# Performance work log

Measured on AMD Instinct MI355X. Metric: run time of the kernel, lower is better.

Reference implementation:

```python
import jax, jax.numpy as jnp
import numpy as np

N_NODES = 110
C = 4096  # in_channels = hidden = out_channels


def setup_inputs() -> dict:
    key = jax.random.key(0)
    ks = jax.random.split(key, 8)
    x = jax.random.normal(ks[0], (N_NODES, C), dtype=jnp.float32)
    adj = jax.random.randint(ks[1], (N_NODES, N_NODES), 0, 2, dtype=jnp.int32)
    # torch.nn.Linear weights stored [out_features, in_features]
    W2 = jax.random.normal(ks[2], (C, C), dtype=jnp.float32) / np.sqrt(C)
    b2 = jax.random.normal(ks[3], (C,), dtype=jnp.float32) * 0.01
    W1 = jax.random.normal(ks[4], (2 * C, C), dtype=jnp.float32) / np.sqrt(2 * C)
    b1 = jax.random.normal(ks[5], (C,), dtype=jnp.float32) * 0.01
    Wl = jax.random.normal(ks[6], (N_NODES, N_NODES), dtype=jnp.float32) / np.sqrt(N_NODES)
    bl = jax.random.normal(ks[7], (N_NODES,), dtype=jnp.float32) * 0.01
    # note: W1 is stored [in=2C, out=C]; W2 [in=C, out=C]; Wl [in=110, out=110]
    return {"x": x, "adj": adj, "W2": W2, "b2": b2, "W1": W1, "b1": b1, "Wl": Wl, "bl": bl}


def reference(x, adj, W2, b2, W1, b1, Wl, bl):
    # FeatGraphConv: h = lin2(x)
    h = x @ W2 + b2  # [N, C]
    # edge_index.nonzero(): adjacency -> edge list (i=src, j=dst); mean-aggregate
    # h[src] at dst. Dense equivalent: column-normalized mask matmul.
    mask = (adj != 0).astype(x.dtype)  # [N, N]
    deg = mask.sum(axis=0)  # in-degree of each target node j
    aggr = (mask.T @ h) / jnp.maximum(deg, 1.0)[:, None]  # [N, C]; 0 for isolated nodes (PyG mean)
    # update: lin1(cat(h, aggr)) then relu (in RegGNN.forward)
    out = jax.nn.relu(jnp.concatenate([h, aggr], axis=1) @ W1 + b1)  # [N, C]
    # x.t(); lin(110,110); x.t()
    out = (out.T @ Wl.T + bl).T  # [N, C]
    return out
```

## Files before the change

kernel.cpp:

```cpp
#include <hip/hip_runtime.h>
#include <hip/hip_fp16.h>

#define C 4096
#define NN 110
#define MPAD 112
#define NMT 7
#define KBS (NMT * 512)
#define NSLICE 8

typedef _Float16 f16x8 __attribute__((ext_vector_type(8)));
typedef float fx4 __attribute__((ext_vector_type(4)));
typedef unsigned long long ull;


__global__ __launch_bounds__(256)
void prep1_kernel(const float* __restrict__ x, _Float16* __restrict__ A1t) {
    int u = blockIdx.x * 256 + threadIdx.x;
    int kb  = u / 448;
    int rem = u - kb * 448;
    int mt  = rem >> 6;
    int L   = rem & 63;
    int n   = mt * 16 + (L & 15);
    int c   = kb * 32 + (L >> 4) * 8;
    f16x8 hv;
    if (n < NN) {
        float4 v0 = *(const float4*)(x + (size_t)n * C + c);
        float4 v1 = *(const float4*)(x + (size_t)n * C + c + 4);
        hv[0]=(_Float16)v0.x; hv[1]=(_Float16)v0.y; hv[2]=(_Float16)v0.z; hv[3]=(_Float16)v0.w;
        hv[4]=(_Float16)v1.x; hv[5]=(_Float16)v1.y; hv[6]=(_Float16)v1.z; hv[7]=(_Float16)v1.w;
    } else {
        for (int e = 0; e < 8; ++e) hv[e] = (_Float16)0.f;
    }
    *(f16x8*)(A1t + (size_t)u * 8) = hv;
}

__global__ __launch_bounds__(128)
void maskprep_kernel(const int* __restrict__ adj, ull* __restrict__ mlo,
                     ull* __restrict__ mhi, float* __restrict__ degs) {
    int j = threadIdx.x;
    if (j < NN) {
        ull lo = 0, hi = 0; int dg = 0;
        for (int i = 0; i < 64; ++i) {
            int m = (adj[i * NN + j] != 0);
            lo |= ((ull)m) << i; dg += m;
        }
        for (int i = 64; i < NN; ++i) {
            int m = (adj[i * NN + j] != 0);
            hi |= ((ull)m) << (i - 64); dg += m;
        }
        mlo[j] = lo; mhi[j] = hi;
        degs[j] = (float)(dg > 0 ? dg : 1);
    }
}

#define PIPE_BARRIER()                                                \
    do {                                                              \
        asm volatile("s_waitcnt lgkmcnt(0)" ::: "memory");            \
        __builtin_amdgcn_s_barrier();                                 \
        __builtin_amdgcn_sched_barrier(0);                            \
    } while (0)

template<int NITER>
__global__ __launch_bounds__(256, 3)
void mm_kernel(const _Float16* __restrict__ A, const float* __restrict__ B,
               float* __restrict__ Cpart) {
    __shared__ __align__(16) _Float16 As[2][2 * KBS];
    __shared__ __align__(16) _Float16 Bs[2][64 * 64];

    const int t   = threadIdx.x;
    const int j0  = blockIdx.x * 64;
    const int w   = t >> 6;
    const int L   = t & 63;
    const int l15 = L & 15;
    const int q   = L >> 4;
    const int sc2 = (t & 31) * 2;
    const int kgr = (t >> 5) & 7;

    fx4 acc[7];
#pragma unroll
    for (int mt = 0; mt < 7; ++mt) acc[mt] = (fx4){0.f, 0.f, 0.f, 0.f};

    const float*    Bp  = B + (size_t)blockIdx.y * (NITER * 64) * C + j0 + sc2;
    const _Float16* ApC = A + (size_t)blockIdx.y * (NITER * 2) * KBS;
    const _Float16* BsR = &Bs[0][0] + (w * 16 + l15) * 64;
    const _Float16* AsR = &As[0][0];

    f16x8  av[4];
    float2 bva[8], bvb[8];

#define LOADA(ch)                                                              \
    { _Pragma("unroll")                                                        \
      for (int i = 0; i < 4; ++i)                                              \
          if (i < 3 || t < 128)                                                \
              av[i] = *(const f16x8*)(ApC + (size_t)(ch) * (2 * KBS)           \
                                      + (t + i * 256) * 8); }

#define COMMITA(buf)                                                           \
    { _Pragma("unroll")                                                        \
      for (int i = 0; i < 4; ++i)                                              \
          if (i < 3 || t < 128)                                                \
              *(f16x8*)(&As[buf][0] + (t + i * 256) * 8) = av[i]; }

#define LOADB(dst, ch)                                                         \
    { _Pragma("unroll")                                                        \
      for (int p = 0; p < 8; ++p)                                              \
          dst[p] = *(const float2*)(Bp + (size_t)((ch) * 64 + kgr * 8 + p) * C); }

#define COMMITB(src, buf)                                                      \
    { f16x8 h0, h1;                                                            \
      _Pragma("unroll")                                                        \
      for (int e = 0; e < 8; ++e) { h0[e] = (_Float16)src[e].x;                \
                                    h1[e] = (_Float16)src[e].y; }              \
      *(f16x8*)(&Bs[buf][0] + sc2 * 64 + ((kgr ^ (sc2 & 7)) << 3)) = h0;       \
      *(f16x8*)(&Bs[buf][0] + (sc2 + 1) * 64 + ((kgr ^ ((sc2 + 1) & 7)) << 3)) = h1; }

    LOADA(0);
    LOADB(bva, 0);
    COMMITA(0);
    COMMITB(bva, 0);
    LOADB(bva, 1);
    PIPE_BARRIER();

#pragma unroll
    for (int it = 0; it < NITER; ++it) {
        if (it + 1 < NITER) LOADA(it + 1);
        __builtin_amdgcn_sched_barrier(0);
        if (it + 2 < NITER) {
            if (it & 1) { LOADB(bva, it + 2); } else { LOADB(bvb, it + 2); }
        }
        __builtin_amdgcn_sched_barrier(0);
#pragma unroll
        for (int s = 0; s < 2; ++s) {
            f16x8 bf = *(const f16x8*)(BsR + (it & 1) * 4096
                            + ((((s << 2) + q) ^ (l15 & 7)) << 3));
#pragma unroll
            for (int mt = 0; mt < 7; ++mt) {
                f16x8 afrag = *(const f16x8*)(AsR + (it & 1) * (2 * KBS)
                                  + (s * 7 + mt) * 512 + L * 8);
                acc[mt] = __builtin_amdgcn_mfma_f32_16x16x32_f16(
                    afrag, bf, acc[mt], 0, 0, 0);
            }
        }
        if (it + 1 < NITER) {
            COMMITA((it + 1) & 1);
            if (it & 1) { COMMITB(bvb, (it + 1) & 1); }
            else        { COMMITB(bva, (it + 1) & 1); }
            PIPE_BARRIER();
        }
    }

    float* Cp = Cpart + (size_t)blockIdx.y * (NN * C) + j0 + w * 16 + l15;
#pragma unroll
    for (int mt = 0; mt < 7; ++mt)
#pragma unroll
        for (int r = 0; r < 4; ++r) {
            int row = mt * 16 + q * 4 + r;
            if (row < NN)
                Cp[(size_t)row * C] = acc[mt][r];
        }
#undef LOADA
#undef COMMITA
#undef LOADB
#undef COMMITB
}

__device__ __forceinline__ size_t fragidx(int n, int c) {
    return (size_t)(c >> 5) * KBS + (n >> 4) * 512
         + (((c >> 3) & 3) * 16 + (n & 15)) * 8 + (c & 7);
}

__global__ __launch_bounds__(256)
void agg_kernel(const float* __restrict__ hpart, const ull* __restrict__ gmlo,
                const ull* __restrict__ gmhi, const float* __restrict__ gdegs,
                const float* __restrict__ b2, _Float16* __restrict__ A3t) {
    __shared__ float hb[NN * 16];
    const int t  = threadIdx.x;
    const int c0 = blockIdx.x * 16;

    for (int idx = t; idx < NN * 8; idx += 256) {
        int n = idx >> 3, cp = (idx & 7) << 1;
        float v0 = b2[c0 + cp], v1 = b2[c0 + cp + 1];
#pragma unroll
        for (int p = 0; p < NSLICE; ++p) {
            float2 v = *(const float2*)(hpart + (size_t)p * (NN * C)
                                        + (size_t)n * C + c0 + cp);
            v0 += v.x; v1 += v.y;
        }
        hb[n * 16 + cp]     = v0;
        hb[n * 16 + cp + 1] = v1;
        union { _Float16 h[2]; unsigned u; } pk;
        pk.h[0] = (_Float16)v0;
        pk.h[1] = (_Float16)v1;
        *(unsigned*)(A3t + fragidx(n, c0 + cp)) = pk.u;
    }
    if (t < 32) {
        int n  = 110 + ((t >> 3) & 1);
        int hs = t >> 4;
        int cp = (t & 7) << 1;
        *(unsigned*)(A3t + fragidx(n, hs * C + c0 + cp)) = 0u;
    }
    __syncthreads();
    for (int idx = t; idx < NN * 8; idx += 256) {
        int j = idx >> 3, cp = (idx & 7) << 1;
        ull lo = gmlo[j], hi = gmhi[j];
        float dg = gdegs[j];
        float a0 = 0.f, a1 = 0.f;
        for (int i = 0; i < 64; ++i)
            if ((lo >> i) & 1) { a0 += hb[i * 16 + cp]; a1 += hb[i * 16 + cp + 1]; }
        for (int i = 64; i < NN; ++i)
            if ((hi >> (i - 64)) & 1) { a0 += hb[i * 16 + cp]; a1 += hb[i * 16 + cp + 1]; }
        union { _Float16 h[2]; unsigned u; } pk;
        pk.h[0] = (_Float16)(a0 / dg);
        pk.h[1] = (_Float16)(a1 / dg);
        *(unsigned*)(A3t + fragidx(j, C + c0 + cp)) = pk.u;
    }
}

__global__ __launch_bounds__(256)
void zred_kernel(const float* __restrict__ zpart, float* __restrict__ z_raw) {
    int idx = blockIdx.x * 256 + threadIdx.x;
    if (idx < NN * (C / 4)) {
        fx4 s = (fx4){0.f, 0.f, 0.f, 0.f};
#pragma unroll
        for (int p = 0; p < NSLICE; ++p) {
            fx4 v = *(const fx4*)(zpart + (size_t)p * (NN * C) + (size_t)idx * 4);
            s.x += v.x; s.y += v.y; s.z += v.z; s.w += v.w;
        }
        *(fx4*)(z_raw + (size_t)idx * 4) = s;
    }
}

__global__ __launch_bounds__(256)
void fin_kernel(const float* __restrict__ z_raw, const float* __restrict__ b1,
                const float* __restrict__ Wl, const float* __restrict__ bl,
                float* __restrict__ out) {
    __shared__ float zs[NN * 64];
    const int t  = threadIdx.x;
    const int c0 = blockIdx.x * 64;
    const int c  = t & 63;

    for (int idx = t; idx < NN * 64; idx += 256) {
        int k = idx >> 6, cc = idx & 63;
        float v = z_raw[(size_t)k * C + c0 + cc] + b1[c0 + cc];
        zs[idx] = fmaxf(v, 0.f);
    }
    __syncthreads();
    for (int jj = 0; jj < 7; ++jj) {
        int j = blockIdx.y * 28 + jj * 4 + (t >> 6);
        if (j < NN) {
            float a = bl[j];
#pragma unroll 2
            for (int k = 0; k < NN; ++k)
                a += Wl[j * NN + k] * zs[k * 64 + c];
            out[(size_t)j * C + c0 + c] = a;
        }
    }
}

extern "C" void kernel_launch(void* const* d_in, const int* in_sizes, int n_in,
                              void* d_out, int out_size, void* d_ws, size_t ws_size,
                              hipStream_t stream) {
    const float* x   = (const float*)d_in[0];
    const int*   adj = (const int*)d_in[1];
    const float* W2  = (const float*)d_in[2];
    const float* b2  = (const float*)d_in[3];
    const float* W1  = (const float*)d_in[4];
    const float* b1  = (const float*)d_in[5];
    const float* Wl  = (const float*)d_in[6];
    const float* bl  = (const float*)d_in[7];
    float* out = (float*)d_out;

    char* ws = (char*)d_ws;
    float*    hpart = (float*)(ws);
    float*    zpart = (float*)(ws + 14417920);
    float*    z_raw = (float*)(ws + 28835840);
    _Float16* A1t   = (_Float16*)(ws + 30638080);
    _Float16* A3t   = (_Float16*)(ws + 31555584);
    ull*      mlo   = (ull*)(ws + 33390592);
    ull*      mhi   = (ull*)(ws + 33391472);
    float*    degs  = (float*)(ws + 33392352);

    prep1_kernel<<<224, 256, 0, stream>>>(x, A1t);
    maskprep_kernel<<<1, 128, 0, stream>>>(adj, mlo, mhi, degs);
    mm_kernel<8><<<dim3(64, NSLICE), 256, 0, stream>>>(A1t, W2, hpart);
    agg_kernel<<<C / 16, 256, 0, stream>>>(hpart, mlo, mhi, degs, b2, A3t);
    mm_kernel<16><<<dim3(64, NSLICE), 256, 0, stream>>>(A3t, W1, zpart);
    zred_kernel<<<440, 256, 0, stream>>>(zpart, z_raw);
    fin_kernel<<<dim3(C / 64, 4), 256, 0, stream>>>(z_raw, b1, Wl, bl, out);
}
```

Before: 352.1 us.

## Load A fragments directly into registers and fuse mask prep into prep1

The mm kernel no longer stages the A operand through shared memory. Each lane now loads its MFMA A fragments straight from global memory into a double-buffered register array, which removes the LDS writes and reads for A. The launch bound occupancy hint drops from 3 to 2 to make room for the larger register footprint. Separately, the adjacency mask preparation moves into an extra block of prep1, saving one kernel launch. The trade-off is heavier global load traffic per wave, since A fragments are reloaded by each of the 4 waves, plus higher register pressure and possibly lower occupancy.

```diff
diff --git a/kernel.cpp b/kernel.cpp
--- a/kernel.cpp
+++ b/kernel.cpp
@@ -14,7 +14,26 @@
 
 
 __global__ __launch_bounds__(256)
-void prep1_kernel(const float* __restrict__ x, _Float16* __restrict__ A1t) {
+void prep1_kernel(const float* __restrict__ x, _Float16* __restrict__ A1t,
+                  const int* __restrict__ adj, ull* __restrict__ mlo,
+                  ull* __restrict__ mhi, float* __restrict__ degs) {
+    if (blockIdx.x == 224) {
+        int j = threadIdx.x;
+        if (j < NN) {
+            ull lo = 0, hi = 0; int dg = 0;
+            for (int i = 0; i < 64; ++i) {
+                int m = (adj[i * NN + j] != 0);
+                lo |= ((ull)m) << i; dg += m;
+            }
+            for (int i = 64; i < NN; ++i) {
+                int m = (adj[i * NN + j] != 0);
+                hi |= ((ull)m) << (i - 64); dg += m;
+            }
+            mlo[j] = lo; mhi[j] = hi;
+            degs[j] = (float)(dg > 0 ? dg : 1);
+        }
+        return;
+    }
     int u = blockIdx.x * 256 + threadIdx.x;
     int kb  = u / 448;
     int rem = u - kb * 448;
@@ -34,25 +53,6 @@
     *(f16x8*)(A1t + (size_t)u * 8) = hv;
 }
 
-__global__ __launch_bounds__(128)
-void maskprep_kernel(const int* __restrict__ adj, ull* __restrict__ mlo,
-                     ull* __restrict__ mhi, float* __restrict__ degs) {
-    int j = threadIdx.x;
-    if (j < NN) {
-        ull lo = 0, hi = 0; int dg = 0;
-        for (int i = 0; i < 64; ++i) {
-            int m = (adj[i * NN + j] != 0);
-            lo |= ((ull)m) << i; dg += m;
-        }
-        for (int i = 64; i < NN; ++i) {
-            int m = (adj[i * NN + j] != 0);
-            hi |= ((ull)m) << (i - 64); dg += m;
-        }
-        mlo[j] = lo; mhi[j] = hi;
-        degs[j] = (float)(dg > 0 ? dg : 1);
-    }
-}
-
 #define PIPE_BARRIER()                                                \
     do {                                                              \
         asm volatile("s_waitcnt lgkmcnt(0)" ::: "memory");            \
@@ -61,10 +61,9 @@
     } while (0)
 
 template<int NITER>
-__global__ __launch_bounds__(256, 3)
+__global__ __launch_bounds__(256, 2)
 void mm_kernel(const _Float16* __restrict__ A, const float* __restrict__ B,
                float* __restrict__ Cpart) {
-    __shared__ __align__(16) _Float16 As[2][2 * KBS];
     __shared__ __align__(16) _Float16 Bs[2][64 * 64];
 
     const int t   = threadIdx.x;
@@ -81,25 +80,19 @@
     for (int mt = 0; mt < 7; ++mt) acc[mt] = (fx4){0.f, 0.f, 0.f, 0.f};
 
     const float*    Bp  = B + (size_t)blockIdx.y * (NITER * 64) * C + j0 + sc2;
-    const _Float16* ApC = A + (size_t)blockIdx.y * (NITER * 2) * KBS;
+    const _Float16* ApL = A + (size_t)blockIdx.y * (NITER * 2) * KBS + L * 8;
     const _Float16* BsR = &Bs[0][0] + (w * 16 + l15) * 64;
-    const _Float16* AsR = &As[0][0];
-
-    f16x8  av[4];
+
+    f16x8  af[2][2][7];
     float2 bva[8], bvb[8];
 
-#define LOADA(ch)                                                              \
+#define LOADAF(buf, ch)                                                        \
     { _Pragma("unroll")                                                        \
-      for (int i = 0; i < 4; ++i)                                              \
-          if (i < 3 || t < 128)                                                \
-              av[i] = *(const f16x8*)(ApC + (size_t)(ch) * (2 * KBS)           \
-                                      + (t + i * 256) * 8); }
-
-#define COMMITA(buf)                                                           \
-    { _Pragma("unroll")                                                        \
-      for (int i = 0; i < 4; ++i)                                              \
-          if (i < 3 || t < 128)                                                \
-              *(f16x8*)(&As[buf][0] + (t + i * 256) * 8) = av[i]; }
+      for (int s = 0; s < 2; ++s)                                              \
+          _Pragma("unroll")                                                    \
+          for (int mt = 0; mt < 7; ++mt)                                       \
+              af[buf][s][mt] = *(const f16x8*)(ApL                             \
+                  + (size_t)((ch) * 2 + s) * KBS + mt * 512); }
 
 #define LOADB(dst, ch)                                                         \
     { _Pragma("unroll")                                                        \
@@ -114,16 +107,15 @@
       *(f16x8*)(&Bs[buf][0] + sc2 * 64 + ((kgr ^ (sc2 & 7)) << 3)) = h0;       \
       *(f16x8*)(&Bs[buf][0] + (sc2 + 1) * 64 + ((kgr ^ ((sc2 + 1) & 7)) << 3)) = h1; }
 
-    LOADA(0);
+    LOADAF(0, 0);
     LOADB(bva, 0);
-    COMMITA(0);
     COMMITB(bva, 0);
     LOADB(bva, 1);
     PIPE_BARRIER();
 
 #pragma unroll
     for (int it = 0; it < NITER; ++it) {
-        if (it + 1 < NITER) LOADA(it + 1);
+        if (it + 1 < NITER) LOADAF((it + 1) & 1, it + 1);
         __builtin_amdgcn_sched_barrier(0);
         if (it + 2 < NITER) {
             if (it & 1) { LOADB(bva, it + 2); } else { LOADB(bvb, it + 2); }
@@ -134,15 +126,11 @@
             f16x8 bf = *(const f16x8*)(BsR + (it & 1) * 4096
                             + ((((s << 2) + q) ^ (l15 & 7)) << 3));
 #pragma unroll
-            for (int mt = 0; mt < 7; ++mt) {
-                f16x8 afrag = *(const f16x8*)(AsR + (it & 1) * (2 * KBS)
-                                  + (s * 7 + mt) * 512 + L * 8);
+            for (int mt = 0; mt < 7; ++mt)
                 acc[mt] = __builtin_amdgcn_mfma_f32_16x16x32_f16(
-                    afrag, bf, acc[mt], 0, 0, 0);
-            }
+                    af[it & 1][s][mt], bf, acc[mt], 0, 0, 0);
         }
         if (it + 1 < NITER) {
-            COMMITA((it + 1) & 1);
             if (it & 1) { COMMITB(bvb, (it + 1) & 1); }
             else        { COMMITB(bva, (it + 1) & 1); }
             PIPE_BARRIER();
@@ -158,8 +146,7 @@
             if (row < NN)
                 Cp[(size_t)row * C] = acc[mt][r];
         }
-#undef LOADA
-#undef COMMITA
+#undef LOADAF
 #undef LOADB
 #undef COMMITB
 }
@@ -280,8 +267,7 @@
     ull*      mhi   = (ull*)(ws + 33391472);
     float*    degs  = (float*)(ws + 33392352);
 
-    prep1_kernel<<<224, 256, 0, stream>>>(x, A1t);
-    maskprep_kernel<<<1, 128, 0, stream>>>(adj, mlo, mhi, degs);
+    prep1_kernel<<<225, 256, 0, stream>>>(x, A1t, adj, mlo, mhi, degs);
     mm_kernel<8><<<dim3(64, NSLICE), 256, 0, stream>>>(A1t, W2, hpart);
     agg_kernel<<<C / 16, 256, 0, stream>>>(hpart, mlo, mhi, degs, b2, A3t);
     mm_kernel<16><<<dim3(64, NSLICE), 256, 0, stream>>>(A3t, W1, zpart);
```

Result: no change. 347.8 us (-1.2%).
